# Kernel tuning notes

Hardware: AMD Instinct MI355X
Metric: run time of the kernel (lower is better)

## Reference

```python
import jax, jax.numpy as jnp
import numpy as np

EPS = 1e-8

def setup_inputs() -> dict:
    key = jax.random.key(0)
    k1, k2 = jax.random.split(key)
    N, C, S = 2000000, 32, 8
    feats = jax.random.normal(k1, (N, C), dtype=jnp.float32)
    seg_ids = jnp.sort(jax.random.randint(k2, (N,), 0, S, dtype=jnp.int32))
    weight = jnp.ones((1, C), dtype=jnp.float32)
    bias = jnp.zeros((1, C), dtype=jnp.float32)
    return {"feats": feats, "seg_ids": seg_ids, "weight": weight, "bias": bias, "num_segments": S}

def reference(feats, seg_ids, weight, bias, num_segments):
    # Per-instance (segment) mean: GlobalPoolingForward with average=True
    counts = jax.ops.segment_sum(jnp.ones((feats.shape[0], 1), feats.dtype), seg_ids,
                                 num_segments=num_segments)  # [S,1]
    counts = jnp.maximum(counts, 1.0)
    mean = jax.ops.segment_sum(feats, seg_ids, num_segments=num_segments) / counts  # [S,C]
    # BroadcastForward ADDITION with -mean
    centered = feats - mean[seg_ids]  # [N,C]
    # Second global pooling: per-instance variance
    var = jax.ops.segment_sum(centered * centered, seg_ids, num_segments=num_segments) / counts  # [S,C]
    inv_std = jax.lax.rsqrt(var + EPS)  # [S,C]
    # BroadcastForward MULTIPLICATION with inv_std, then affine
    norm = centered * inv_std[seg_ids]
    return norm * weight + bias
```

## Files before the change

### kernel.cpp

```cpp
#include <hip/hip_runtime.h>
#include <math.h>


#define NSH      8
#define SHARD_F  4160
#define WS_SCALE (NSH * SHARD_F)
#define WS_SHIFT (WS_SCALE + 2048)

#define NB    4
#define STEPS 32

typedef float f32x4 __attribute__((ext_vector_type(4)));

typedef const __attribute__((address_space(1))) unsigned int ga_u32;
typedef __attribute__((address_space(3))) unsigned int la_u32;
#define GLL16(gp, lp) \
    __builtin_amdgcn_global_load_lds((ga_u32*)(gp), (la_u32*)(lp), 16, 0, 0)

__global__ __launch_bounds__(256) void zero_ws_kernel(float* __restrict__ ws) {
    int t = blockIdx.x * blockDim.x + threadIdx.x;
    if (t < NSH * SHARD_F) ws[t] = 0.0f;
}

__global__ __launch_bounds__(256) void reduce_kernel(
        const float* __restrict__ feats, const int* __restrict__ seg,
        float* __restrict__ ws, int total4, int N) {
    __shared__ __align__(16) char dma[4 * NB * 1024];
    __shared__ float s_sum[2048];
    __shared__ float s_sq[2048];
    __shared__ float s_cnt[64];
    int t = threadIdx.x;
    for (int j = t; j < 2048; j += 256) { s_sum[j] = 0.0f; s_sq[j] = 0.0f; }
    if (t < 64) s_cnt[t] = 0.0f;
    __syncthreads();

    int wid  = t >> 6;
    int lane = t & 63;
    int cg   = lane & 7;
    const f32x4* f4 = (const f32x4*)feats;
    long ebase = ((long)blockIdx.x * 4 + wid) * 2048;

    if (ebase < total4) {
        long eend = ebase + 2048;
        if (eend > total4) eend = total4;
        int row0 = (int)(ebase >> 3);
        int row1 = (int)((eend - 1) >> 3);
        int sA = seg[row0];
        int sB = seg[row1];
        f32x4 acc  = {0.f, 0.f, 0.f, 0.f};
        f32x4 accq = {0.f, 0.f, 0.f, 0.f};

        if (sA == sB && (eend - ebase) == 2048) {
            const char* g = (const char*)(f4 + ebase) + lane * 16;
            char* lb = &dma[wid * (NB * 1024)];
            asm volatile("s_waitcnt vmcnt(0)" ::: "memory");
            #pragma unroll
            for (int k = 0; k < NB; ++k)
                GLL16(g + k * 1024, lb + k * 1024);
            for (int k = 0; k < STEPS - NB; ++k) {
                asm volatile("s_waitcnt vmcnt(3)" ::: "memory");
                __builtin_amdgcn_sched_barrier(0);
                f32x4 v = *(const f32x4*)(lb + (k & (NB - 1)) * 1024 + lane * 16);
                acc  += v;
                accq += v * v;
                __builtin_amdgcn_sched_barrier(0);
                GLL16(g + (k + NB) * 1024, lb + (k & (NB - 1)) * 1024);
            }
            asm volatile("s_waitcnt vmcnt(0)" ::: "memory");
            __builtin_amdgcn_sched_barrier(0);
            #pragma unroll
            for (int k = STEPS - NB; k < STEPS; ++k) {
                f32x4 v = *(const f32x4*)(lb + (k & (NB - 1)) * 1024 + lane * 16);
                acc  += v;
                accq += v * v;
            }
            #pragma unroll
            for (int m = 8; m <= 32; m <<= 1) {
                acc.x  += __shfl_xor(acc.x, m);  acc.y  += __shfl_xor(acc.y, m);
                acc.z  += __shfl_xor(acc.z, m);  acc.w  += __shfl_xor(acc.w, m);
                accq.x += __shfl_xor(accq.x, m); accq.y += __shfl_xor(accq.y, m);
                accq.z += __shfl_xor(accq.z, m); accq.w += __shfl_xor(accq.w, m);
            }
            if (lane < 8) {
                int bse = sA * 32 + lane * 4;
                atomicAdd(&s_sum[bse + 0], acc.x);
                atomicAdd(&s_sum[bse + 1], acc.y);
                atomicAdd(&s_sum[bse + 2], acc.z);
                atomicAdd(&s_sum[bse + 3], acc.w);
                atomicAdd(&s_sq[bse + 0], accq.x);
                atomicAdd(&s_sq[bse + 1], accq.y);
                atomicAdd(&s_sq[bse + 2], accq.z);
                atomicAdd(&s_sq[bse + 3], accq.w);
            }
            if (lane == 0) atomicAdd(&s_cnt[sA], 256.0f);
        } else {
            for (long e = ebase + lane; e < eend; e += 64) {
                int s = seg[(int)(e >> 3)];
                f32x4 v = f4[e];
                int bse = s * 32 + cg * 4;
                atomicAdd(&s_sum[bse + 0], v.x);
                atomicAdd(&s_sum[bse + 1], v.y);
                atomicAdd(&s_sum[bse + 2], v.z);
                atomicAdd(&s_sum[bse + 3], v.w);
                atomicAdd(&s_sq[bse + 0], v.x * v.x);
                atomicAdd(&s_sq[bse + 1], v.y * v.y);
                atomicAdd(&s_sq[bse + 2], v.z * v.z);
                atomicAdd(&s_sq[bse + 3], v.w * v.w);
                if (cg == 0) atomicAdd(&s_cnt[s], 1.0f);
            }
        }
    }
    __syncthreads();

    float* shard = ws + (blockIdx.x & (NSH - 1)) * SHARD_F;
    for (int j = t; j < 2048; j += 256) {
        float a = s_sum[j];
        float q = s_sq[j];
        if (a != 0.0f) atomicAdd(&shard[j], a);
        if (q != 0.0f) atomicAdd(&shard[2048 + j], q);
    }
    if (t < 64) {
        float c = s_cnt[t];
        if (c != 0.0f) atomicAdd(&shard[4096 + t], c);
    }
}

__global__ void stats_kernel(const float* __restrict__ w,
                             const float* __restrict__ b,
                             const int* __restrict__ nsp,
                             float* __restrict__ ws) {
    int t  = threadIdx.x;
    int ns = min(*nsp, 64);
    for (int o = t; o < ns * 32; o += 256) {
        int s = o >> 5, c = o & 31;
        float S = 0.f, Q = 0.f, C = 0.f;
        #pragma unroll
        for (int sh = 0; sh < NSH; ++sh) {
            const float* base = ws + sh * SHARD_F;
            S += base[o];
            Q += base[2048 + o];
            C += base[4096 + s];
        }
        float cnt  = fmaxf(C, 1.0f);
        float mean = S / cnt;
        float var  = fmaxf(Q / cnt - mean * mean, 0.0f);
        float inv  = rsqrtf(var + 1e-8f);
        float sc   = inv * w[c];
        ws[WS_SCALE + o] = sc;
        ws[WS_SHIFT + o] = b[c] - mean * sc;
    }
}

__global__ __launch_bounds__(256) void apply_kernel(
        const float* __restrict__ feats, const int* __restrict__ seg,
        const float* __restrict__ ws, float* __restrict__ out, int total4) {
    const f32x4* f4 = (const f32x4*)feats;
    f32x4*       o4 = (f32x4*)out;
    const f32x4* scale4 = (const f32x4*)(ws + WS_SCALE);
    const f32x4* shift4 = (const f32x4*)(ws + WS_SHIFT);
    int stride = gridDim.x * blockDim.x;
    for (int i = blockIdx.x * blockDim.x + threadIdx.x; i < total4; i += stride) {
        int row = i >> 3, cg = i & 7;
        int s = seg[row];
        f32x4 v  = f4[i];
        f32x4 sc = scale4[s * 8 + cg];
        f32x4 sh = shift4[s * 8 + cg];
        f32x4 o;
        o.x = fmaf(v.x, sc.x, sh.x); o.y = fmaf(v.y, sc.y, sh.y);
        o.z = fmaf(v.z, sc.z, sh.z); o.w = fmaf(v.w, sc.w, sh.w);
        __builtin_nontemporal_store(o, &o4[i]);
    }
}

extern "C" void kernel_launch(void* const* d_in, const int* in_sizes, int n_in,
                              void* d_out, int out_size, void* d_ws, size_t ws_size,
                              hipStream_t stream) {
    const float* feats = (const float*)d_in[0];
    const int*   seg   = (const int*)d_in[1];
    const float* w     = (const float*)d_in[2];
    const float* b     = (const float*)d_in[3];
    const int*   nsp   = (const int*)d_in[4];
    float* out = (float*)d_out;
    float* ws  = (float*)d_ws;

    int N = in_sizes[1];
    int total4 = N * 8;
    int nwaves = (total4 + 2047) / 2048;
    int nblk_r = (nwaves + 3) / 4;

    hipLaunchKernelGGL(zero_ws_kernel, dim3((NSH * SHARD_F + 255) / 256), dim3(256),
                       0, stream, ws);
    hipLaunchKernelGGL(reduce_kernel, dim3(nblk_r), dim3(256), 0, stream,
                       feats, seg, ws, total4, N);
    hipLaunchKernelGGL(stats_kernel, dim3(1), dim3(256), 0, stream,
                       w, b, nsp, ws);
    hipLaunchKernelGGL(apply_kernel, dim3(4096), dim3(256), 0, stream,
                       feats, seg, ws, out, total4);
}
```

Baseline: 148.4 us.

## Restructure apply kernel into per-wave chunks with LDS-staged async loads

The apply pass now gives each wave a contiguous chunk of 2048 float4s, the same chunking the reduce kernel uses. When a chunk lies inside one segment, the scale and shift are loaded once per lane, and the features are streamed through an LDS ring buffer with global_load_lds and manual vmcnt waits. This removes the per-element segment-id and scale/shift gathers and is meant to keep more loads in flight. Chunks that span a segment boundary fall back to a per-element loop. The grid now scales with the data instead of a fixed grid-stride launch, and the hand-tuned waitcnt counts must correctly account for the interleaved stores.

```diff
diff --git a/kernel.cpp b/kernel.cpp
--- a/kernel.cpp
+++ b/kernel.cpp
@@ -154,21 +154,76 @@
 __global__ __launch_bounds__(256) void apply_kernel(
         const float* __restrict__ feats, const int* __restrict__ seg,
         const float* __restrict__ ws, float* __restrict__ out, int total4) {
+    __shared__ __align__(16) char dma[4 * NB * 1024];
+    int t    = threadIdx.x;
+    int wid  = t >> 6;
+    int lane = t & 63;
+    int cg   = lane & 7;
     const f32x4* f4 = (const f32x4*)feats;
     f32x4*       o4 = (f32x4*)out;
     const f32x4* scale4 = (const f32x4*)(ws + WS_SCALE);
     const f32x4* shift4 = (const f32x4*)(ws + WS_SHIFT);
-    int stride = gridDim.x * blockDim.x;
-    for (int i = blockIdx.x * blockDim.x + threadIdx.x; i < total4; i += stride) {
-        int row = i >> 3, cg = i & 7;
-        int s = seg[row];
-        f32x4 v  = f4[i];
-        f32x4 sc = scale4[s * 8 + cg];
-        f32x4 sh = shift4[s * 8 + cg];
-        f32x4 o;
-        o.x = fmaf(v.x, sc.x, sh.x); o.y = fmaf(v.y, sc.y, sh.y);
-        o.z = fmaf(v.z, sc.z, sh.z); o.w = fmaf(v.w, sc.w, sh.w);
-        __builtin_nontemporal_store(o, &o4[i]);
+
+    long ebase = ((long)blockIdx.x * 4 + wid) * 2048;
+    if (ebase >= total4) return;
+    long eend = ebase + 2048;
+    if (eend > total4) eend = total4;
+    int sA = seg[(int)(ebase >> 3)];
+    int sB = seg[(int)((eend - 1) >> 3)];
+
+    if (sA == sB && (eend - ebase) == 2048) {
+        f32x4 sc = scale4[sA * 8 + cg];
+        f32x4 sh = shift4[sA * 8 + cg];
+        const char* g = (const char*)(f4 + ebase) + lane * 16;
+        char* lb = &dma[wid * (NB * 1024)];
+        asm volatile("s_waitcnt vmcnt(0)" ::: "memory");
+        #pragma unroll
+        for (int k = 0; k < NB; ++k)
+            GLL16(g + k * 1024, lb + k * 1024);
+        #pragma unroll
+        for (int k = 0; k < NB; ++k) {
+            asm volatile("s_waitcnt vmcnt(3)" ::: "memory");
+            __builtin_amdgcn_sched_barrier(0);
+            f32x4 v = *(const f32x4*)(lb + (k & (NB - 1)) * 1024 + lane * 16);
+            f32x4 o;
+            o.x = fmaf(v.x, sc.x, sh.x); o.y = fmaf(v.y, sc.y, sh.y);
+            o.z = fmaf(v.z, sc.z, sh.z); o.w = fmaf(v.w, sc.w, sh.w);
+            __builtin_nontemporal_store(o, &o4[ebase + k * 64 + lane]);
+            __builtin_amdgcn_sched_barrier(0);
+            GLL16(g + (k + NB) * 1024, lb + (k & (NB - 1)) * 1024);
+        }
+        for (int k = NB; k < STEPS - NB; ++k) {
+            asm volatile("s_waitcnt vmcnt(6)" ::: "memory");
+            __builtin_amdgcn_sched_barrier(0);
+            f32x4 v = *(const f32x4*)(lb + (k & (NB - 1)) * 1024 + lane * 16);
+            f32x4 o;
+            o.x = fmaf(v.x, sc.x, sh.x); o.y = fmaf(v.y, sc.y, sh.y);
+            o.z = fmaf(v.z, sc.z, sh.z); o.w = fmaf(v.w, sc.w, sh.w);
+            __builtin_nontemporal_store(o, &o4[ebase + k * 64 + lane]);
+            __builtin_amdgcn_sched_barrier(0);
+            GLL16(g + (k + NB) * 1024, lb + (k & (NB - 1)) * 1024);
+        }
+        asm volatile("s_waitcnt vmcnt(0)" ::: "memory");
+        __builtin_amdgcn_sched_barrier(0);
+        #pragma unroll
+        for (int k = STEPS - NB; k < STEPS; ++k) {
+            f32x4 v = *(const f32x4*)(lb + (k & (NB - 1)) * 1024 + lane * 16);
+            f32x4 o;
+            o.x = fmaf(v.x, sc.x, sh.x); o.y = fmaf(v.y, sc.y, sh.y);
+            o.z = fmaf(v.z, sc.z, sh.z); o.w = fmaf(v.w, sc.w, sh.w);
+            __builtin_nontemporal_store(o, &o4[ebase + k * 64 + lane]);
+        }
+    } else {
+        for (long e = ebase + lane; e < eend; e += 64) {
+            int s = seg[(int)(e >> 3)];
+            f32x4 v  = f4[e];
+            f32x4 sc = scale4[s * 8 + cg];
+            f32x4 sh = shift4[s * 8 + cg];
+            f32x4 o;
+            o.x = fmaf(v.x, sc.x, sh.x); o.y = fmaf(v.y, sc.y, sh.y);
+            o.z = fmaf(v.z, sc.z, sh.z); o.w = fmaf(v.w, sc.w, sh.w);
+            __builtin_nontemporal_store(o, &o4[e]);
+        }
     }
 }
 
@@ -194,6 +249,6 @@
                        feats, seg, ws, total4, N);
     hipLaunchKernelGGL(stats_kernel, dim3(1), dim3(256), 0, stream,
                        w, b, nsp, ws);
-    hipLaunchKernelGGL(apply_kernel, dim3(4096), dim3(256), 0, stream,
+    hipLaunchKernelGGL(apply_kernel, dim3(nblk_r), dim3(256), 0, stream,
                        feats, seg, ws, out, total4);
 }
```

New measurement: 148.7 us. About the same (+0.2%).

## Enlarge per-wave reduce chunk, drop LDS staging, atomically accumulate wave partials to global

Applied to the files above, without the earlier changes.

Each wave now reduces 8192 float4s (128 steps) with an 8-deep global-to-LDS prefetch ring instead of 2048 with a 4-deep ring. The shared-memory per-block histogram and its block-wide syncs are removed, so each wave adds its partial sums straight to a global shard with atomics. Boundary chunks now split by segment using binary search and register accumulation instead of per-element LDS atomics. This cuts grid size, LDS zero-init, barriers and flush overhead, in exchange for more global atomics per wave and fewer waves to hide memory latency.

```diff
diff --git a/kernel.cpp b/kernel.cpp
--- a/kernel.cpp
+++ b/kernel.cpp
@@ -7,8 +7,8 @@
 #define WS_SCALE (NSH * SHARD_F)
 #define WS_SHIFT (WS_SCALE + 2048)
 
-#define NB    4
-#define STEPS 32
+#define NB    8
+#define STEPS 128
 
 typedef float f32x4 __attribute__((ext_vector_type(4)));
 
@@ -22,106 +22,104 @@
     if (t < NSH * SHARD_F) ws[t] = 0.0f;
 }
 
+__device__ inline int lower_bound(const int* __restrict__ a, int n, int key) {
+    int lo = 0, hi = n;
+    while (lo < hi) {
+        int mid = (lo + hi) >> 1;
+        if (a[mid] < key) lo = mid + 1; else hi = mid;
+    }
+    return lo;
+}
+
 __global__ __launch_bounds__(256) void reduce_kernel(
         const float* __restrict__ feats, const int* __restrict__ seg,
         float* __restrict__ ws, int total4, int N) {
     __shared__ __align__(16) char dma[4 * NB * 1024];
-    __shared__ float s_sum[2048];
-    __shared__ float s_sq[2048];
-    __shared__ float s_cnt[64];
-    int t = threadIdx.x;
-    for (int j = t; j < 2048; j += 256) { s_sum[j] = 0.0f; s_sq[j] = 0.0f; }
-    if (t < 64) s_cnt[t] = 0.0f;
-    __syncthreads();
-
+    int t    = threadIdx.x;
     int wid  = t >> 6;
     int lane = t & 63;
-    int cg   = lane & 7;
     const f32x4* f4 = (const f32x4*)feats;
-    long ebase = ((long)blockIdx.x * 4 + wid) * 2048;
 
-    if (ebase < total4) {
-        long eend = ebase + 2048;
-        if (eend > total4) eend = total4;
-        int row0 = (int)(ebase >> 3);
-        int row1 = (int)((eend - 1) >> 3);
-        int sA = seg[row0];
-        int sB = seg[row1];
+    long gw    = (long)blockIdx.x * 4 + wid;
+    long ebase = gw * (STEPS * 64);
+    if (ebase >= total4) return;
+    long eend = ebase + STEPS * 64;
+    if (eend > total4) eend = total4;
+    int sA = seg[(int)(ebase >> 3)];
+    int sB = seg[(int)((eend - 1) >> 3)];
+    float* shard = ws + ((int)gw & (NSH - 1)) * SHARD_F;
+
+    if (sA == sB && (eend - ebase) == STEPS * 64) {
         f32x4 acc  = {0.f, 0.f, 0.f, 0.f};
         f32x4 accq = {0.f, 0.f, 0.f, 0.f};
-
-        if (sA == sB && (eend - ebase) == 2048) {
-            const char* g = (const char*)(f4 + ebase) + lane * 16;
-            char* lb = &dma[wid * (NB * 1024)];
-            asm volatile("s_waitcnt vmcnt(0)" ::: "memory");
-            #pragma unroll
-            for (int k = 0; k < NB; ++k)
-                GLL16(g + k * 1024, lb + k * 1024);
-            for (int k = 0; k < STEPS - NB; ++k) {
-                asm volatile("s_waitcnt vmcnt(3)" ::: "memory");
-                __builtin_amdgcn_sched_barrier(0);
-                f32x4 v = *(const f32x4*)(lb + (k & (NB - 1)) * 1024 + lane * 16);
+        const char* g = (const char*)(f4 + ebase) + lane * 16;
+        char* lb = &dma[wid * (NB * 1024)];
+        asm volatile("s_waitcnt vmcnt(0)" ::: "memory");
+        #pragma unroll
+        for (int k = 0; k < NB; ++k)
+            GLL16(g + k * 1024, lb + k * 1024);
+        for (int k = 0; k < STEPS - NB; ++k) {
+            asm volatile("s_waitcnt vmcnt(7)" ::: "memory");
+            __builtin_amdgcn_sched_barrier(0);
+            f32x4 v = *(const f32x4*)(lb + (k & (NB - 1)) * 1024 + lane * 16);
+            acc  += v;
+            accq += v * v;
+            __builtin_amdgcn_sched_barrier(0);
+            GLL16(g + (k + NB) * 1024, lb + (k & (NB - 1)) * 1024);
+        }
+        asm volatile("s_waitcnt vmcnt(0)" ::: "memory");
+        __builtin_amdgcn_sched_barrier(0);
+        #pragma unroll
+        for (int k = STEPS - NB; k < STEPS; ++k) {
+            f32x4 v = *(const f32x4*)(lb + (k & (NB - 1)) * 1024 + lane * 16);
+            acc  += v;
+            accq += v * v;
+        }
+        #pragma unroll
+        for (int m = 8; m <= 32; m <<= 1) {
+            acc.x  += __shfl_xor(acc.x, m);  acc.y  += __shfl_xor(acc.y, m);
+            acc.z  += __shfl_xor(acc.z, m);  acc.w  += __shfl_xor(acc.w, m);
+            accq.x += __shfl_xor(accq.x, m); accq.y += __shfl_xor(accq.y, m);
+            accq.z += __shfl_xor(accq.z, m); accq.w += __shfl_xor(accq.w, m);
+        }
+        if (lane < 8) {
+            int bse = sA * 32 + lane * 4;
+            atomicAdd(&shard[bse + 0], acc.x);
+            atomicAdd(&shard[bse + 1], acc.y);
+            atomicAdd(&shard[bse + 2], acc.z);
+            atomicAdd(&shard[bse + 3], acc.w);
+            atomicAdd(&shard[2048 + bse + 0], accq.x);
+            atomicAdd(&shard[2048 + bse + 1], accq.y);
+            atomicAdd(&shard[2048 + bse + 2], accq.z);
+            atomicAdd(&shard[2048 + bse + 3], accq.w);
+        }
+        if (lane == 0) atomicAdd(&shard[4096 + sA], (float)(STEPS * 64 / 8));
+    } else {
+        for (int s = sA; s <= sB; ++s) {
+            long lo = (s == sA) ? ebase : (long)lower_bound(seg, N, s) * 8;
+            long hi = (s == sB) ? eend  : (long)lower_bound(seg, N, s + 1) * 8;
+            if (hi <= lo) continue;
+            f32x4 acc  = {0.f, 0.f, 0.f, 0.f};
+            f32x4 accq = {0.f, 0.f, 0.f, 0.f};
+            float rcnt = 0.0f;
+            int cg_s = (int)((lo + lane) & 7);
+            for (long e = lo + lane; e < hi; e += 64) {
+                f32x4 v = f4[e];
                 acc  += v;
                 accq += v * v;
-                __builtin_amdgcn_sched_barrier(0);
-                GLL16(g + (k + NB) * 1024, lb + (k & (NB - 1)) * 1024);
+                rcnt += (cg_s == 0) ? 1.0f : 0.0f;
             }
-            asm volatile("s_waitcnt vmcnt(0)" ::: "memory");
-            __builtin_amdgcn_sched_barrier(0);
-            #pragma unroll
-            for (int k = STEPS - NB; k < STEPS; ++k) {
-                f32x4 v = *(const f32x4*)(lb + (k & (NB - 1)) * 1024 + lane * 16);
-                acc  += v;
-                accq += v * v;
-            }
-            #pragma unroll
-            for (int m = 8; m <= 32; m <<= 1) {
-                acc.x  += __shfl_xor(acc.x, m);  acc.y  += __shfl_xor(acc.y, m);
-                acc.z  += __shfl_xor(acc.z, m);  acc.w  += __shfl_xor(acc.w, m);
-                accq.x += __shfl_xor(accq.x, m); accq.y += __shfl_xor(accq.y, m);
-                accq.z += __shfl_xor(accq.z, m); accq.w += __shfl_xor(accq.w, m);
-            }
-            if (lane < 8) {
-                int bse = sA * 32 + lane * 4;
-                atomicAdd(&s_sum[bse + 0], acc.x);
-                atomicAdd(&s_sum[bse + 1], acc.y);
-                atomicAdd(&s_sum[bse + 2], acc.z);
-                atomicAdd(&s_sum[bse + 3], acc.w);
-                atomicAdd(&s_sq[bse + 0], accq.x);
-                atomicAdd(&s_sq[bse + 1], accq.y);
-                atomicAdd(&s_sq[bse + 2], accq.z);
-                atomicAdd(&s_sq[bse + 3], accq.w);
-            }
-            if (lane == 0) atomicAdd(&s_cnt[sA], 256.0f);
-        } else {
-            for (long e = ebase + lane; e < eend; e += 64) {
-                int s = seg[(int)(e >> 3)];
-                f32x4 v = f4[e];
-                int bse = s * 32 + cg * 4;
-                atomicAdd(&s_sum[bse + 0], v.x);
-                atomicAdd(&s_sum[bse + 1], v.y);
-                atomicAdd(&s_sum[bse + 2], v.z);
-                atomicAdd(&s_sum[bse + 3], v.w);
-                atomicAdd(&s_sq[bse + 0], v.x * v.x);
-                atomicAdd(&s_sq[bse + 1], v.y * v.y);
-                atomicAdd(&s_sq[bse + 2], v.z * v.z);
-                atomicAdd(&s_sq[bse + 3], v.w * v.w);
-                if (cg == 0) atomicAdd(&s_cnt[s], 1.0f);
-            }
+            int bse = s * 32 + cg_s * 4;
+            atomicAdd(&shard[bse + 0], acc.x);
+            atomicAdd(&shard[bse + 1], acc.y);
+            atomicAdd(&shard[bse + 2], acc.z);
+            atomicAdd(&shard[bse + 3], acc.w);
+            atomicAdd(&shard[2048 + bse + 0], accq.x);
+            atomicAdd(&shard[2048 + bse + 1], accq.y);
+            atomicAdd(&shard[2048 + bse + 2], accq.z);
+            atomicAdd(&shard[2048 + bse + 3], accq.w);
+            if (rcnt != 0.0f) atomicAdd(&shard[4096 + s], rcnt);
         }
-    }
-    __syncthreads();
-
-    float* shard = ws + (blockIdx.x & (NSH - 1)) * SHARD_F;
-    for (int j = t; j < 2048; j += 256) {
-        float a = s_sum[j];
-        float q = s_sq[j];
-        if (a != 0.0f) atomicAdd(&shard[j], a);
-        if (q != 0.0f) atomicAdd(&shard[2048 + j], q);
-    }
-    if (t < 64) {
-        float c = s_cnt[t];
-        if (c != 0.0f) atomicAdd(&shard[4096 + t], c);
     }
 }
 
@@ -185,7 +183,7 @@
 
     int N = in_sizes[1];
     int total4 = N * 8;
-    int nwaves = (total4 + 2047) / 2048;
+    int nwaves = (total4 + STEPS * 64 - 1) / (STEPS * 64);
     int nblk_r = (nwaves + 3) / 4;
 
     hipLaunchKernelGGL(zero_ws_kernel, dim3((NSH * SHARD_F + 255) / 256), dim3(256),
```

Measured after the change: 170.9 us. 15.2% more time.

## Fuse stats into reduce via last-block ticket and prefetch before LDS zeroing

Applied to the files above, without the earlier changes.

Removes the separate single-block stats kernel launch. The block that draws the final value from a global atomic ticket computes the per-segment scale and shift inside the reduce kernel. It also issues the initial global-to-LDS loads before zeroing the shared accumulators, so the memory latency overlaps that setup. In exchange, every block now pays a threadfence and a ticket atomic, and correctness relies on fence ordering across blocks.

```diff
diff --git a/kernel.cpp b/kernel.cpp
--- a/kernel.cpp
+++ b/kernel.cpp
@@ -6,6 +6,7 @@
 #define SHARD_F  4160
 #define WS_SCALE (NSH * SHARD_F)
 #define WS_SHIFT (WS_SCALE + 2048)
+#define WS_TICKET (WS_SHIFT + 2048)
 
 #define NB    4
 #define STEPS 32
@@ -19,44 +20,55 @@
 
 __global__ __launch_bounds__(256) void zero_ws_kernel(float* __restrict__ ws) {
     int t = blockIdx.x * blockDim.x + threadIdx.x;
-    if (t < NSH * SHARD_F) ws[t] = 0.0f;
+    if (t < NSH * SHARD_F + 1) ws[t < NSH * SHARD_F ? t : WS_TICKET] = 0.0f;
 }
 
 __global__ __launch_bounds__(256) void reduce_kernel(
         const float* __restrict__ feats, const int* __restrict__ seg,
-        float* __restrict__ ws, int total4, int N) {
+        const float* __restrict__ w, const float* __restrict__ b,
+        const int* __restrict__ nsp, float* __restrict__ ws,
+        int total4, int N, int nblk) {
     __shared__ __align__(16) char dma[4 * NB * 1024];
     __shared__ float s_sum[2048];
     __shared__ float s_sq[2048];
     __shared__ float s_cnt[64];
-    int t = threadIdx.x;
-    for (int j = t; j < 2048; j += 256) { s_sum[j] = 0.0f; s_sq[j] = 0.0f; }
-    if (t < 64) s_cnt[t] = 0.0f;
-    __syncthreads();
-
+    __shared__ int   s_last;
+
+    int t    = threadIdx.x;
     int wid  = t >> 6;
     int lane = t & 63;
     int cg   = lane & 7;
     const f32x4* f4 = (const f32x4*)feats;
     long ebase = ((long)blockIdx.x * 4 + wid) * 2048;
 
-    if (ebase < total4) {
-        long eend = ebase + 2048;
-        if (eend > total4) eend = total4;
-        int row0 = (int)(ebase >> 3);
-        int row1 = (int)((eend - 1) >> 3);
-        int sA = seg[row0];
-        int sB = seg[row1];
+    bool active = ebase < total4;
+    long eend = ebase + 2048;
+    if (eend > total4) eend = total4;
+    int sA = 0, sB = 0;
+    bool fastp = false;
+    if (active) {
+        sA = seg[(int)(ebase >> 3)];
+        sB = seg[(int)((eend - 1) >> 3)];
+        fastp = (sA == sB) && ((eend - ebase) == 2048);
+    }
+
+    const char* g = (const char*)(f4 + ebase) + lane * 16;
+    char* lb = &dma[wid * (NB * 1024)];
+    if (fastp) {
+        asm volatile("s_waitcnt vmcnt(0)" ::: "memory");
+        #pragma unroll
+        for (int k = 0; k < NB; ++k)
+            GLL16(g + k * 1024, lb + k * 1024);
+    }
+
+    for (int j = t; j < 2048; j += 256) { s_sum[j] = 0.0f; s_sq[j] = 0.0f; }
+    if (t < 64) s_cnt[t] = 0.0f;
+    __syncthreads();
+
+    if (active) {
         f32x4 acc  = {0.f, 0.f, 0.f, 0.f};
         f32x4 accq = {0.f, 0.f, 0.f, 0.f};
-
-        if (sA == sB && (eend - ebase) == 2048) {
-            const char* g = (const char*)(f4 + ebase) + lane * 16;
-            char* lb = &dma[wid * (NB * 1024)];
-            asm volatile("s_waitcnt vmcnt(0)" ::: "memory");
-            #pragma unroll
-            for (int k = 0; k < NB; ++k)
-                GLL16(g + k * 1024, lb + k * 1024);
+        if (fastp) {
             for (int k = 0; k < STEPS - NB; ++k) {
                 asm volatile("s_waitcnt vmcnt(3)" ::: "memory");
                 __builtin_amdgcn_sched_barrier(0);
@@ -123,31 +135,35 @@
         float c = s_cnt[t];
         if (c != 0.0f) atomicAdd(&shard[4096 + t], c);
     }
-}
-
-__global__ void stats_kernel(const float* __restrict__ w,
-                             const float* __restrict__ b,
-                             const int* __restrict__ nsp,
-                             float* __restrict__ ws) {
-    int t  = threadIdx.x;
-    int ns = min(*nsp, 64);
-    for (int o = t; o < ns * 32; o += 256) {
-        int s = o >> 5, c = o & 31;
-        float S = 0.f, Q = 0.f, C = 0.f;
-        #pragma unroll
-        for (int sh = 0; sh < NSH; ++sh) {
-            const float* base = ws + sh * SHARD_F;
-            S += base[o];
-            Q += base[2048 + o];
-            C += base[4096 + s];
+
+    __threadfence();
+    __syncthreads();
+    if (t == 0) {
+        unsigned int ticket = atomicAdd((unsigned int*)(ws + WS_TICKET), 1u);
+        s_last = (ticket == (unsigned int)(nblk - 1));
+    }
+    __syncthreads();
+    if (s_last) {
+        __threadfence();
+        int ns = min(*nsp, 64);
+        for (int o = t; o < ns * 32; o += 256) {
+            int s = o >> 5, c = o & 31;
+            float S = 0.f, Q = 0.f, C = 0.f;
+            #pragma unroll
+            for (int sh = 0; sh < NSH; ++sh) {
+                const float* base = ws + sh * SHARD_F;
+                S += base[o];
+                Q += base[2048 + o];
+                C += base[4096 + s];
+            }
+            float cnt  = fmaxf(C, 1.0f);
+            float mean = S / cnt;
+            float var  = fmaxf(Q / cnt - mean * mean, 0.0f);
+            float inv  = rsqrtf(var + 1e-8f);
+            float sc   = inv * w[c];
+            ws[WS_SCALE + o] = sc;
+            ws[WS_SHIFT + o] = b[c] - mean * sc;
         }
-        float cnt  = fmaxf(C, 1.0f);
-        float mean = S / cnt;
-        float var  = fmaxf(Q / cnt - mean * mean, 0.0f);
-        float inv  = rsqrtf(var + 1e-8f);
-        float sc   = inv * w[c];
-        ws[WS_SCALE + o] = sc;
-        ws[WS_SHIFT + o] = b[c] - mean * sc;
     }
 }
 
@@ -188,12 +204,10 @@
     int nwaves = (total4 + 2047) / 2048;
     int nblk_r = (nwaves + 3) / 4;
 
-    hipLaunchKernelGGL(zero_ws_kernel, dim3((NSH * SHARD_F + 255) / 256), dim3(256),
+    hipLaunchKernelGGL(zero_ws_kernel, dim3((NSH * SHARD_F + 256) / 256), dim3(256),
                        0, stream, ws);
     hipLaunchKernelGGL(reduce_kernel, dim3(nblk_r), dim3(256), 0, stream,
-                       feats, seg, ws, total4, N);
-    hipLaunchKernelGGL(stats_kernel, dim3(1), dim3(256), 0, stream,
-                       w, b, nsp, ws);
+                       feats, seg, w, b, nsp, ws, total4, N, nblk_r);
     hipLaunchKernelGGL(apply_kernel, dim3(4096), dim3(256), 0, stream,
                        feats, seg, ws, out, total4);
 }
```

After: 274.5 us. +85.0%, slower.
